# Kernel optimization log

Hardware: AMD Instinct MI355X
Metric: run time of the kernel (lower is better)

Reference implementation:

```python
import jax, jax.numpy as jnp
import numpy as np
from jax import lax

G0, G1 = 16, 16
UNITS = 256


def setup_inputs() -> dict:
    key = jax.random.key(0)
    ks = jax.random.split(key, 20)
    B, H, W, C = 64, 512, 512, 3
    U = UNITS
    flat = 12 * 12 * 3  # after two VALID 3x3 convs on 16x16x3
    inp = {
        'image': jax.random.normal(ks[0], (B, H, W, C), jnp.float32),
        'section': jax.random.uniform(ks[1], (B, 3), jnp.float32),
        'h0': jax.random.normal(ks[2], (B, U), jnp.float32) * 0.1,
        'c0': jax.random.normal(ks[3], (B, U), jnp.float32) * 0.1,
        'conv1_k': jax.random.normal(ks[4], (3, 3, C, 3), jnp.float32) * 0.2,
        'conv1_b': jnp.zeros((3,), jnp.float32),
        'conv2_k': jax.random.normal(ks[5], (3, 3, 3, 3), jnp.float32) * 0.2,
        'conv2_b': jnp.zeros((3,), jnp.float32),
        'dense_w': jax.random.normal(ks[6], (flat, U), jnp.float32) * (1.0 / np.sqrt(flat)),
        'dense_b': jnp.zeros((U,), jnp.float32),
        'lstm_k': jax.random.normal(ks[7], (U, 4 * U), jnp.float32) * (1.0 / np.sqrt(U)),
        'lstm_rk': jax.random.normal(ks[8], (U, 4 * U), jnp.float32) * (1.0 / np.sqrt(U)),
        'lstm_b': jnp.zeros((4 * U,), jnp.float32),
        'nsc_w1': jax.random.normal(ks[9], (U, U), jnp.float32) * (1.0 / np.sqrt(U)),
        'nsc_b1': jnp.zeros((U,), jnp.float32),
        'nsc_w2': jax.random.normal(ks[10], (U, 3), jnp.float32) * (1.0 / np.sqrt(U)),
        'nsc_b2': jnp.zeros((3,), jnp.float32),
    }
    return inp


def _interpolate(image, section):
    # image: (B,H,W,C); section: (B,3) = (x, y, scale); coords in [0,1],
    # mapped linearly onto grid indices with constant (clamp) extension,
    # matching tfp.math.batch_interp_regular_nd_grid over image axes 1,2.
    B, H, W, C = image.shape
    starts = section[:, :2]                       # (B,2)
    stops = section[:, :2] + section[:, 2:]       # (B,2) broadcast scale
    t0 = jnp.linspace(0.0, 1.0, G0)               # along grid_dim[0]
    alpha = jnp.linspace(0.0, 1.0, G1)            # along grid_dim[1]
    # p0[b,i,j]: coordinate mapped to image axis 1 (H)
    p0 = (starts[:, 0, None] + t0[None, :] * (stops[:, 0] - starts[:, 0])[:, None])[:, :, None]
    p0 = jnp.broadcast_to(p0, (B, G0, G1))
    # p1[b,i,j]: coordinate mapped to image axis 2 (W)
    p1 = (starts[:, 1, None] + alpha[None, :] * (stops[:, 1] - starts[:, 1])[:, None])[:, None, :]
    p1 = jnp.broadcast_to(p1, (B, G0, G1))
    fy = jnp.clip(p0 * (H - 1), 0.0, H - 1)
    fx = jnp.clip(p1 * (W - 1), 0.0, W - 1)
    y0 = jnp.floor(fy).astype(jnp.int32)
    x0 = jnp.floor(fx).astype(jnp.int32)
    y1 = jnp.minimum(y0 + 1, H - 1)
    x1 = jnp.minimum(x0 + 1, W - 1)
    wy = (fy - y0)[..., None]
    wx = (fx - x0)[..., None]
    b = jnp.arange(B)[:, None, None]
    v00 = image[b, y0, x0]
    v01 = image[b, y0, x1]
    v10 = image[b, y1, x0]
    v11 = image[b, y1, x1]
    top = v00 * (1 - wx) + v01 * wx
    bot = v10 * (1 - wx) + v11 * wx
    return top * (1 - wy) + bot * wy            # (B,G0,G1,C)


def _conv_relu(x, k, b):
    y = lax.conv_general_dilated(x, k, (1, 1), 'VALID',
                                 dimension_numbers=('NHWC', 'HWIO', 'NHWC'))
    return jax.nn.relu(y + b)


def reference(image, section, h0, c0, conv1_k, conv1_b, conv2_k, conv2_b,
              dense_w, dense_b, lstm_k, lstm_rk, lstm_b,
              nsc_w1, nsc_b1, nsc_w2, nsc_b2):
    sec = _interpolate(image, section)                 # (B,16,16,C)
    x = _conv_relu(sec, conv1_k, conv1_b)              # (B,14,14,3)
    x = _conv_relu(x, conv2_k, conv2_b)                # (B,12,12,3)
    x = x.reshape(x.shape[0], -1)                      # (B,432)
    x = jax.nn.relu(x @ dense_w + dense_b)             # (B,U)
    # Keras LSTMCell: gate order i, f, g(c), o
    z = x @ lstm_k + h0 @ lstm_rk + lstm_b
    i, f, g, o = jnp.split(z, 4, axis=-1)
    c_new = jax.nn.sigmoid(f) * c0 + jax.nn.sigmoid(i) * jnp.tanh(g)
    h_new = jax.nn.sigmoid(o) * jnp.tanh(c_new)
    nsc = jax.nn.relu(h_new @ nsc_w1 + nsc_b1)
    next_section = jax.nn.sigmoid(nsc @ nsc_w2 + nsc_b2)  # (B,3)
    return h_new, c_new, next_section
```

## Files before the change

kernel.cpp:

```cpp
#include <hip/hip_runtime.h>
#include <math.h>

#define BATCH 64
#define IMH 512
#define IMW 512
#define UNITS 256

__device__ __forceinline__ float sigmoidf_(float x) {
    return 1.0f / (1.0f + __expf(-x));
}
__device__ __forceinline__ float tanhf_(float x) {
    float e = __expf(2.0f * x);
    return 1.0f - 2.0f / (e + 1.0f);
}

#define WS_X   0
#define WS_Z   16384
#define WS_NSC (16384 + 65536)

__global__ __launch_bounds__(512) void k1_front(
    const float* __restrict__ image, const float* __restrict__ section,
    const float* __restrict__ k1, const float* __restrict__ b1,
    const float* __restrict__ k2, const float* __restrict__ b2,
    const float* __restrict__ dw, const float* __restrict__ db,
    float* __restrict__ ws)
{
    const int b   = blockIdx.x;
    const int tid = threadIdx.x;

    __shared__ float s_sec[16][16][3];
    __shared__ float s_c1[14][14][3];
    __shared__ float s_flat[432];
    __shared__ float s_pf[2048];
    __shared__ float s_k1[84];
    __shared__ float s_k2[84];

    if (tid < 81)       s_k1[tid]      = k1[tid];
    else if (tid < 84)  s_k1[tid]      = b1[tid - 81];
    else if (tid < 165) s_k2[tid - 84] = k2[tid - 84];
    else if (tid < 168) s_k2[tid - 84] = b2[tid - 165];

    if (tid < 256) {
        const float s0 = section[b * 3 + 0];
        const float s1 = section[b * 3 + 1];
        const float s2 = section[b * 3 + 2];
        const int i = tid >> 4, j = tid & 15;
        float p0 = s0 + (float)i * (1.0f / 15.0f) * s2;
        float p1 = s1 + (float)j * (1.0f / 15.0f) * s2;
        float fy = fminf(fmaxf(p0 * 511.0f, 0.0f), 511.0f);
        float fx = fminf(fmaxf(p1 * 511.0f, 0.0f), 511.0f);
        int y0 = (int)floorf(fy);
        int x0 = (int)floorf(fx);
        int y1 = min(y0 + 1, 511);
        int x1 = min(x0 + 1, 511);
        float wy = fy - (float)y0;
        float wx = fx - (float)x0;
        const float* base = image + (size_t)b * IMH * IMW * 3;
        const float* p00 = base + (y0 * IMW + x0) * 3;
        const float* p01 = base + (y0 * IMW + x1) * 3;
        const float* p10 = base + (y1 * IMW + x0) * 3;
        const float* p11 = base + (y1 * IMW + x1) * 3;
        #pragma unroll
        for (int c = 0; c < 3; ++c) {
            float top = p00[c] * (1.0f - wx) + p01[c] * wx;
            float bot = p10[c] * (1.0f - wx) + p11[c] * wx;
            s_sec[i][j][c] = top * (1.0f - wy) + bot * wy;
        }
    }
    __syncthreads();

    if (tid < 196) {
        const int i = tid / 14, j = tid % 14;
        float a0 = s_k1[81], a1 = s_k1[82], a2 = s_k1[83];
        #pragma unroll
        for (int di = 0; di < 3; ++di)
            #pragma unroll
            for (int dj = 0; dj < 3; ++dj)
                #pragma unroll
                for (int ci = 0; ci < 3; ++ci) {
                    float v = s_sec[i + di][j + dj][ci];
                    const int kb = ((di * 3 + dj) * 3 + ci) * 3;
                    a0 += v * s_k1[kb + 0];
                    a1 += v * s_k1[kb + 1];
                    a2 += v * s_k1[kb + 2];
                }
        s_c1[i][j][0] = fmaxf(a0, 0.0f);
        s_c1[i][j][1] = fmaxf(a1, 0.0f);
        s_c1[i][j][2] = fmaxf(a2, 0.0f);
    }
    __syncthreads();

    if (tid < 144) {
        const int i = tid / 12, j = tid % 12;
        float a0 = s_k2[81], a1 = s_k2[82], a2 = s_k2[83];
        #pragma unroll
        for (int di = 0; di < 3; ++di)
            #pragma unroll
            for (int dj = 0; dj < 3; ++dj)
                #pragma unroll
                for (int ci = 0; ci < 3; ++ci) {
                    float v = s_c1[i + di][j + dj][ci];
                    const int kb = ((di * 3 + dj) * 3 + ci) * 3;
                    a0 += v * s_k2[kb + 0];
                    a1 += v * s_k2[kb + 1];
                    a2 += v * s_k2[kb + 2];
                }
        const int fb = tid * 3;
        s_flat[fb + 0] = fmaxf(a0, 0.0f);
        s_flat[fb + 1] = fmaxf(a1, 0.0f);
        s_flat[fb + 2] = fmaxf(a2, 0.0f);
    }
    __syncthreads();

    {
        const int ks = tid >> 6;
        const int q  = tid & 63;
        const int k0 = ks * 54;
        const float4* wp = (const float4*)dw + (size_t)k0 * 64 + q;
        const float* fp = s_flat + k0;
        float4 acc = {0.f, 0.f, 0.f, 0.f};
        #pragma unroll 18
        for (int k = 0; k < 54; ++k) {
            const float4 w = wp[k * 64];
            const float v = fp[k];
            acc.x += v * w.x; acc.y += v * w.y; acc.z += v * w.z; acc.w += v * w.w;
        }
        ((float4*)s_pf)[ks * 64 + q] = acc;
    }
    __syncthreads();
    if (tid < 256) {
        const int q2 = tid >> 2, comp = tid & 3;
        float a = db[tid];
        #pragma unroll
        for (int ks2 = 0; ks2 < 8; ++ks2)
            a += s_pf[(ks2 * 64 + q2) * 4 + comp];
        ws[WS_X + b * 256 + tid] = fmaxf(a, 0.0f);
    }
}

__global__ __launch_bounds__(256) void k2_lstm_gemm(
    const float* __restrict__ h0, const float* __restrict__ lk,
    const float* __restrict__ lrk, const float* __restrict__ lb,
    float* __restrict__ ws)
{
    const int bx    = blockIdx.x;
    const int ct    = bx & 15;
    const int bt    = bx >> 4;
    const int col0  = ct * 64;
    const int colq0 = ct * 16;
    const int row0  = bt * 4;
    const int tid   = threadIdx.x;

    __shared__ float s_x4[4][256];
    __shared__ float s_h4[4][256];
    __shared__ float s_zpf[1024];

    for (int i = tid; i < 1024; i += 256) {
        const int r = i >> 8, k = i & 255;
        s_x4[r][k] = ws[WS_X + (row0 + r) * 256 + k];
        s_h4[r][k] = h0[(row0 + r) * 256 + k];
    }
    __syncthreads();

    {
        const int q  = tid & 15;
        const int bb = (tid >> 4) & 3;
        const int ks = tid >> 6;
        const int k0 = ks * 64;
        const float4* lkp = (const float4*)lk  + (size_t)k0 * 256 + colq0 + q;
        const float4* lrp = (const float4*)lrk + (size_t)k0 * 256 + colq0 + q;
        const float* xp = s_x4[bb] + k0;
        const float* hp = s_h4[bb] + k0;
        float4 acc = {0.f, 0.f, 0.f, 0.f};
        #pragma unroll 16
        for (int k = 0; k < 64; ++k) {
            const float4 a = lkp[k * 256];
            const float4 r = lrp[k * 256];
            const float xv = xp[k];
            const float hv = hp[k];
            acc.x += xv * a.x + hv * r.x;
            acc.y += xv * a.y + hv * r.y;
            acc.z += xv * a.z + hv * r.z;
            acc.w += xv * a.w + hv * r.w;
        }
        ((float4*)s_zpf)[(ks * 4 + bb) * 16 + q] = acc;
    }
    __syncthreads();

    {
        const int c   = tid & 63;
        const int bb2 = tid >> 6;
        const int q2 = c >> 2, comp = c & 3;
        float z = lb[col0 + c];
        #pragma unroll
        for (int ks2 = 0; ks2 < 4; ++ks2)
            z += s_zpf[((ks2 * 4 + bb2) * 16 + q2) * 4 + comp];
        ws[WS_Z + (row0 + bb2) * 1024 + col0 + c] = z;
    }
}

__global__ __launch_bounds__(256) void k3_cell_nsc1(
    const float* __restrict__ c0, const float* __restrict__ w1,
    const float* __restrict__ nb1, float* __restrict__ ws,
    float* __restrict__ out)
{
    const int bx    = blockIdx.x;
    const int ct    = bx & 3;
    const int bt    = bx >> 2;
    const int col0  = ct * 64;
    const int colq0 = ct * 16;
    const int row0  = bt * 2;
    const int tid   = threadIdx.x;

    __shared__ float s_hn[2][256];
    __shared__ float s_pf[1024];

    {
        const int u = tid;
        #pragma unroll
        for (int b2 = 0; b2 < 2; ++b2) {
            const int row = row0 + b2;
            const float zi = ws[WS_Z + row * 1024 + u];
            const float zf = ws[WS_Z + row * 1024 + 256 + u];
            const float zg = ws[WS_Z + row * 1024 + 512 + u];
            const float zo = ws[WS_Z + row * 1024 + 768 + u];
            const float cprev = c0[row * 256 + u];
            const float cn = sigmoidf_(zf) * cprev + sigmoidf_(zi) * tanhf_(zg);
            const float hn = sigmoidf_(zo) * tanhf_(cn);
            s_hn[b2][u] = hn;
            if (ct == 0) {
                out[row * 256 + u] = hn;
                out[BATCH * UNITS + row * 256 + u] = cn;
            }
        }
    }
    __syncthreads();

    {
        const int q  = tid & 15;
        const int bb = (tid >> 4) & 1;
        const int ks = tid >> 5;
        const int k0 = ks * 32;
        const float4* wp = (const float4*)w1 + (size_t)k0 * 64 + colq0 + q;
        const float* hp = s_hn[bb] + k0;
        float4 acc = {0.f, 0.f, 0.f, 0.f};
        #pragma unroll 16
        for (int k = 0; k < 32; ++k) {
            const float4 w = wp[k * 64];
            const float v = hp[k];
            acc.x += v * w.x; acc.y += v * w.y; acc.z += v * w.z; acc.w += v * w.w;
        }
        ((float4*)s_pf)[(ks * 2 + bb) * 16 + q] = acc;
    }
    __syncthreads();

    if (tid < 128) {
        const int c   = tid & 63;
        const int bb2 = tid >> 6;
        const int q2 = c >> 2, comp = c & 3;
        float a = nb1[col0 + c];
        #pragma unroll
        for (int ks2 = 0; ks2 < 8; ++ks2)
            a += s_pf[((ks2 * 2 + bb2) * 16 + q2) * 4 + comp];
        ws[WS_NSC + (row0 + bb2) * 256 + col0 + c] = fmaxf(a, 0.0f);
    }
}

__global__ __launch_bounds__(192) void k4_nsc2(
    const float* __restrict__ w2, const float* __restrict__ nb2,
    const float* __restrict__ ws, float* __restrict__ out)
{
    const int b   = blockIdx.x;
    const int tid = threadIdx.x;
    const int j = tid >> 6;
    const int l = tid & 63;
    float p = 0.0f;
    #pragma unroll
    for (int k = l; k < 256; k += 64)
        p += ws[WS_NSC + b * 256 + k] * w2[k * 3 + j];
    #pragma unroll
    for (int off = 32; off > 0; off >>= 1)
        p += __shfl_down(p, off);
    if (l == 0)
        out[2 * BATCH * UNITS + b * 3 + j] = sigmoidf_(p + nb2[j]);
}

extern "C" void kernel_launch(void* const* d_in, const int* in_sizes, int n_in,
                              void* d_out, int out_size, void* d_ws, size_t ws_size,
                              hipStream_t stream) {
    const float* image   = (const float*)d_in[0];
    const float* section = (const float*)d_in[1];
    const float* h0      = (const float*)d_in[2];
    const float* c0      = (const float*)d_in[3];
    const float* k1      = (const float*)d_in[4];
    const float* b1      = (const float*)d_in[5];
    const float* k2      = (const float*)d_in[6];
    const float* b2      = (const float*)d_in[7];
    const float* dw      = (const float*)d_in[8];
    const float* db      = (const float*)d_in[9];
    const float* lk      = (const float*)d_in[10];
    const float* lrk     = (const float*)d_in[11];
    const float* lb      = (const float*)d_in[12];
    const float* w1      = (const float*)d_in[13];
    const float* nb1     = (const float*)d_in[14];
    const float* w2      = (const float*)d_in[15];
    const float* nb2     = (const float*)d_in[16];
    float* out = (float*)d_out;
    float* ws  = (float*)d_ws;

    k1_front<<<64, 512, 0, stream>>>(image, section, k1, b1, k2, b2, dw, db, ws);
    k2_lstm_gemm<<<256, 256, 0, stream>>>(h0, lk, lrk, lb, ws);
    k3_cell_nsc1<<<128, 256, 0, stream>>>(c0, w1, nb1, ws, out);
    k4_nsc2<<<64, 192, 0, stream>>>(w2, nb2, ws, out);
}
```

Before: 302.6 us.

## Fuse four kernels into one cooperative kernel with grid syncs

Replaces the four separate launches (front conv/dense, LSTM GEMM, cell+nsc1, nsc2) with a single cooperative kernel of 256 blocks that uses grid.sync between phases. The cell, nsc1 and nsc2 stages are merged per batch row into one block, so the NSC intermediate stays in shared memory instead of going through the workspace. The front stage now runs with 256 threads instead of 512. The aim is to remove launch overhead and inter-kernel gaps. In exchange it adds grid-wide barrier cost, leaves most blocks idle in the per-batch phases, and the union of shared buffers raises per-block LDS use.

```diff
diff --git a/kernel.cpp b/kernel.cpp
--- a/kernel.cpp
+++ b/kernel.cpp
@@ -1,5 +1,8 @@
 #include <hip/hip_runtime.h>
+#include <hip/hip_cooperative_groups.h>
 #include <math.h>
+
+namespace cg = cooperative_groups;
 
 #define BATCH 64
 #define IMH 512
@@ -14,275 +17,254 @@
     return 1.0f - 2.0f / (e + 1.0f);
 }
 
-#define WS_X   0
-#define WS_Z   16384
-#define WS_NSC (16384 + 65536)
-
-__global__ __launch_bounds__(512) void k1_front(
+#define WS_X 0
+#define WS_Z 16384
+
+__global__ __launch_bounds__(256) void fused_coop(
     const float* __restrict__ image, const float* __restrict__ section,
+    const float* __restrict__ h0, const float* __restrict__ c0,
     const float* __restrict__ k1, const float* __restrict__ b1,
     const float* __restrict__ k2, const float* __restrict__ b2,
     const float* __restrict__ dw, const float* __restrict__ db,
+    const float* __restrict__ lk, const float* __restrict__ lrk,
+    const float* __restrict__ lb, const float* __restrict__ w1,
+    const float* __restrict__ nb1, const float* __restrict__ w2,
+    const float* __restrict__ nb2, float* __restrict__ out,
     float* __restrict__ ws)
 {
-    const int b   = blockIdx.x;
+    cg::grid_group grid = cg::this_grid();
+    const int bx  = blockIdx.x;
     const int tid = threadIdx.x;
 
     __shared__ float s_sec[16][16][3];
     __shared__ float s_c1[14][14][3];
     __shared__ float s_flat[432];
-    __shared__ float s_pf[2048];
     __shared__ float s_k1[84];
     __shared__ float s_k2[84];
-
-    if (tid < 81)       s_k1[tid]      = k1[tid];
-    else if (tid < 84)  s_k1[tid]      = b1[tid - 81];
-    else if (tid < 165) s_k2[tid - 84] = k2[tid - 84];
-    else if (tid < 168) s_k2[tid - 84] = b2[tid - 165];
-
-    if (tid < 256) {
-        const float s0 = section[b * 3 + 0];
-        const float s1 = section[b * 3 + 1];
-        const float s2 = section[b * 3 + 2];
-        const int i = tid >> 4, j = tid & 15;
-        float p0 = s0 + (float)i * (1.0f / 15.0f) * s2;
-        float p1 = s1 + (float)j * (1.0f / 15.0f) * s2;
-        float fy = fminf(fmaxf(p0 * 511.0f, 0.0f), 511.0f);
-        float fx = fminf(fmaxf(p1 * 511.0f, 0.0f), 511.0f);
-        int y0 = (int)floorf(fy);
-        int x0 = (int)floorf(fx);
-        int y1 = min(y0 + 1, 511);
-        int x1 = min(x0 + 1, 511);
-        float wy = fy - (float)y0;
-        float wx = fx - (float)x0;
-        const float* base = image + (size_t)b * IMH * IMW * 3;
-        const float* p00 = base + (y0 * IMW + x0) * 3;
-        const float* p01 = base + (y0 * IMW + x1) * 3;
-        const float* p10 = base + (y1 * IMW + x0) * 3;
-        const float* p11 = base + (y1 * IMW + x1) * 3;
-        #pragma unroll
-        for (int c = 0; c < 3; ++c) {
-            float top = p00[c] * (1.0f - wx) + p01[c] * wx;
-            float bot = p10[c] * (1.0f - wx) + p11[c] * wx;
-            s_sec[i][j][c] = top * (1.0f - wy) + bot * wy;
-        }
-    }
-    __syncthreads();
-
-    if (tid < 196) {
-        const int i = tid / 14, j = tid % 14;
-        float a0 = s_k1[81], a1 = s_k1[82], a2 = s_k1[83];
-        #pragma unroll
-        for (int di = 0; di < 3; ++di)
-            #pragma unroll
-            for (int dj = 0; dj < 3; ++dj)
-                #pragma unroll
-                for (int ci = 0; ci < 3; ++ci) {
-                    float v = s_sec[i + di][j + dj][ci];
-                    const int kb = ((di * 3 + dj) * 3 + ci) * 3;
-                    a0 += v * s_k1[kb + 0];
-                    a1 += v * s_k1[kb + 1];
-                    a2 += v * s_k1[kb + 2];
-                }
-        s_c1[i][j][0] = fmaxf(a0, 0.0f);
-        s_c1[i][j][1] = fmaxf(a1, 0.0f);
-        s_c1[i][j][2] = fmaxf(a2, 0.0f);
-    }
-    __syncthreads();
-
-    if (tid < 144) {
-        const int i = tid / 12, j = tid % 12;
-        float a0 = s_k2[81], a1 = s_k2[82], a2 = s_k2[83];
-        #pragma unroll
-        for (int di = 0; di < 3; ++di)
-            #pragma unroll
-            for (int dj = 0; dj < 3; ++dj)
-                #pragma unroll
-                for (int ci = 0; ci < 3; ++ci) {
-                    float v = s_c1[i + di][j + dj][ci];
-                    const int kb = ((di * 3 + dj) * 3 + ci) * 3;
-                    a0 += v * s_k2[kb + 0];
-                    a1 += v * s_k2[kb + 1];
-                    a2 += v * s_k2[kb + 2];
-                }
-        const int fb = tid * 3;
-        s_flat[fb + 0] = fmaxf(a0, 0.0f);
-        s_flat[fb + 1] = fmaxf(a1, 0.0f);
-        s_flat[fb + 2] = fmaxf(a2, 0.0f);
-    }
-    __syncthreads();
-
-    {
-        const int ks = tid >> 6;
-        const int q  = tid & 63;
-        const int k0 = ks * 54;
-        const float4* wp = (const float4*)dw + (size_t)k0 * 64 + q;
-        const float* fp = s_flat + k0;
-        float4 acc = {0.f, 0.f, 0.f, 0.f};
-        #pragma unroll 18
-        for (int k = 0; k < 54; ++k) {
-            const float4 w = wp[k * 64];
-            const float v = fp[k];
-            acc.x += v * w.x; acc.y += v * w.y; acc.z += v * w.z; acc.w += v * w.w;
-        }
-        ((float4*)s_pf)[ks * 64 + q] = acc;
-    }
-    __syncthreads();
-    if (tid < 256) {
-        const int q2 = tid >> 2, comp = tid & 3;
-        float a = db[tid];
-        #pragma unroll
-        for (int ks2 = 0; ks2 < 8; ++ks2)
-            a += s_pf[(ks2 * 64 + q2) * 4 + comp];
-        ws[WS_X + b * 256 + tid] = fmaxf(a, 0.0f);
-    }
-}
-
-__global__ __launch_bounds__(256) void k2_lstm_gemm(
-    const float* __restrict__ h0, const float* __restrict__ lk,
-    const float* __restrict__ lrk, const float* __restrict__ lb,
-    float* __restrict__ ws)
-{
-    const int bx    = blockIdx.x;
-    const int ct    = bx & 15;
-    const int bt    = bx >> 4;
-    const int col0  = ct * 64;
-    const int colq0 = ct * 16;
-    const int row0  = bt * 4;
-    const int tid   = threadIdx.x;
-
+    __shared__ float s_pf[1024];
     __shared__ float s_x4[4][256];
     __shared__ float s_h4[4][256];
     __shared__ float s_zpf[1024];
-
-    for (int i = tid; i < 1024; i += 256) {
-        const int r = i >> 8, k = i & 255;
-        s_x4[r][k] = ws[WS_X + (row0 + r) * 256 + k];
-        s_h4[r][k] = h0[(row0 + r) * 256 + k];
+    __shared__ float s_hn[256];
+    __shared__ float s_nsc[256];
+
+    if (bx < 64) {
+        const int b = bx;
+
+        if (tid < 81)       s_k1[tid]      = k1[tid];
+        else if (tid < 84)  s_k1[tid]      = b1[tid - 81];
+        else if (tid < 165) s_k2[tid - 84] = k2[tid - 84];
+        else if (tid < 168) s_k2[tid - 84] = b2[tid - 165];
+
+        {
+            const float s0 = section[b * 3 + 0];
+            const float s1 = section[b * 3 + 1];
+            const float s2 = section[b * 3 + 2];
+            const int i = tid >> 4, j = tid & 15;
+            float p0 = s0 + (float)i * (1.0f / 15.0f) * s2;
+            float p1 = s1 + (float)j * (1.0f / 15.0f) * s2;
+            float fy = fminf(fmaxf(p0 * 511.0f, 0.0f), 511.0f);
+            float fx = fminf(fmaxf(p1 * 511.0f, 0.0f), 511.0f);
+            int y0 = (int)floorf(fy);
+            int x0 = (int)floorf(fx);
+            int y1 = min(y0 + 1, 511);
+            int x1 = min(x0 + 1, 511);
+            float wy = fy - (float)y0;
+            float wx = fx - (float)x0;
+            const float* base = image + (size_t)b * IMH * IMW * 3;
+            const float* p00 = base + (y0 * IMW + x0) * 3;
+            const float* p01 = base + (y0 * IMW + x1) * 3;
+            const float* p10 = base + (y1 * IMW + x0) * 3;
+            const float* p11 = base + (y1 * IMW + x1) * 3;
+            #pragma unroll
+            for (int c = 0; c < 3; ++c) {
+                float top = p00[c] * (1.0f - wx) + p01[c] * wx;
+                float bot = p10[c] * (1.0f - wx) + p11[c] * wx;
+                s_sec[i][j][c] = top * (1.0f - wy) + bot * wy;
+            }
+        }
+        __syncthreads();
+
+        if (tid < 196) {
+            const int i = tid / 14, j = tid % 14;
+            float a0 = s_k1[81], a1 = s_k1[82], a2 = s_k1[83];
+            #pragma unroll
+            for (int di = 0; di < 3; ++di)
+                #pragma unroll
+                for (int dj = 0; dj < 3; ++dj)
+                    #pragma unroll
+                    for (int ci = 0; ci < 3; ++ci) {
+                        float v = s_sec[i + di][j + dj][ci];
+                        const int kb = ((di * 3 + dj) * 3 + ci) * 3;
+                        a0 += v * s_k1[kb + 0];
+                        a1 += v * s_k1[kb + 1];
+                        a2 += v * s_k1[kb + 2];
+                    }
+            s_c1[i][j][0] = fmaxf(a0, 0.0f);
+            s_c1[i][j][1] = fmaxf(a1, 0.0f);
+            s_c1[i][j][2] = fmaxf(a2, 0.0f);
+        }
+        __syncthreads();
+
+        if (tid < 144) {
+            const int i = tid / 12, j = tid % 12;
+            float a0 = s_k2[81], a1 = s_k2[82], a2 = s_k2[83];
+            #pragma unroll
+            for (int di = 0; di < 3; ++di)
+                #pragma unroll
+                for (int dj = 0; dj < 3; ++dj)
+                    #pragma unroll
+                    for (int ci = 0; ci < 3; ++ci) {
+                        float v = s_c1[i + di][j + dj][ci];
+                        const int kb = ((di * 3 + dj) * 3 + ci) * 3;
+                        a0 += v * s_k2[kb + 0];
+                        a1 += v * s_k2[kb + 1];
+                        a2 += v * s_k2[kb + 2];
+                    }
+            const int fb = tid * 3;
+            s_flat[fb + 0] = fmaxf(a0, 0.0f);
+            s_flat[fb + 1] = fmaxf(a1, 0.0f);
+            s_flat[fb + 2] = fmaxf(a2, 0.0f);
+        }
+        __syncthreads();
+
+        {
+            const int ks = tid >> 6;
+            const int q  = tid & 63;
+            const int k0 = ks * 108;
+            const float4* wp = (const float4*)dw + (size_t)k0 * 64 + q;
+            const float* fp = s_flat + k0;
+            float4 acc = {0.f, 0.f, 0.f, 0.f};
+            #pragma unroll 27
+            for (int k = 0; k < 108; ++k) {
+                const float4 w = wp[k * 64];
+                const float v = fp[k];
+                acc.x += v * w.x; acc.y += v * w.y; acc.z += v * w.z; acc.w += v * w.w;
+            }
+            ((float4*)s_pf)[ks * 64 + q] = acc;
+        }
+        __syncthreads();
+        {
+            float a = db[tid];
+            #pragma unroll
+            for (int ks2 = 0; ks2 < 4; ++ks2)
+                a += s_pf[ks2 * 256 + tid];
+            ws[WS_X + b * 256 + tid] = fmaxf(a, 0.0f);
+        }
     }
-    __syncthreads();
+
+    grid.sync();
 
     {
-        const int q  = tid & 15;
-        const int bb = (tid >> 4) & 3;
-        const int ks = tid >> 6;
-        const int k0 = ks * 64;
-        const float4* lkp = (const float4*)lk  + (size_t)k0 * 256 + colq0 + q;
-        const float4* lrp = (const float4*)lrk + (size_t)k0 * 256 + colq0 + q;
-        const float* xp = s_x4[bb] + k0;
-        const float* hp = s_h4[bb] + k0;
-        float4 acc = {0.f, 0.f, 0.f, 0.f};
-        #pragma unroll 16
-        for (int k = 0; k < 64; ++k) {
-            const float4 a = lkp[k * 256];
-            const float4 r = lrp[k * 256];
-            const float xv = xp[k];
-            const float hv = hp[k];
-            acc.x += xv * a.x + hv * r.x;
-            acc.y += xv * a.y + hv * r.y;
-            acc.z += xv * a.z + hv * r.z;
-            acc.w += xv * a.w + hv * r.w;
-        }
-        ((float4*)s_zpf)[(ks * 4 + bb) * 16 + q] = acc;
+        const int ct    = bx & 15;
+        const int bt    = bx >> 4;
+        const int col0  = ct * 64;
+        const int colq0 = ct * 16;
+        const int row0  = bt * 4;
+
+        for (int i = tid; i < 1024; i += 256) {
+            const int r = i >> 8, k = i & 255;
+            s_x4[r][k] = ws[WS_X + (row0 + r) * 256 + k];
+            s_h4[r][k] = h0[(row0 + r) * 256 + k];
+        }
+        __syncthreads();
+
+        {
+            const int q  = tid & 15;
+            const int bb = (tid >> 4) & 3;
+            const int ks = tid >> 6;
+            const int k0 = ks * 64;
+            const float4* lkp = (const float4*)lk  + (size_t)k0 * 256 + colq0 + q;
+            const float4* lrp = (const float4*)lrk + (size_t)k0 * 256 + colq0 + q;
+            const float* xp = s_x4[bb] + k0;
+            const float* hp = s_h4[bb] + k0;
+            float4 acc = {0.f, 0.f, 0.f, 0.f};
+            #pragma unroll 16
+            for (int k = 0; k < 64; ++k) {
+                const float4 a = lkp[k * 256];
+                const float4 r = lrp[k * 256];
+                const float xv = xp[k];
+                const float hv = hp[k];
+                acc.x += xv * a.x + hv * r.x;
+                acc.y += xv * a.y + hv * r.y;
+                acc.z += xv * a.z + hv * r.z;
+                acc.w += xv * a.w + hv * r.w;
+            }
+            ((float4*)s_zpf)[(ks * 4 + bb) * 16 + q] = acc;
+        }
+        __syncthreads();
+
+        {
+            const int c   = tid & 63;
+            const int bb2 = tid >> 6;
+            const int q2 = c >> 2, comp = c & 3;
+            float z = lb[col0 + c];
+            #pragma unroll
+            for (int ks2 = 0; ks2 < 4; ++ks2)
+                z += s_zpf[((ks2 * 4 + bb2) * 16 + q2) * 4 + comp];
+            ws[WS_Z + (row0 + bb2) * 1024 + col0 + c] = z;
+        }
     }
-    __syncthreads();
-
-    {
-        const int c   = tid & 63;
-        const int bb2 = tid >> 6;
-        const int q2 = c >> 2, comp = c & 3;
-        float z = lb[col0 + c];
-        #pragma unroll
-        for (int ks2 = 0; ks2 < 4; ++ks2)
-            z += s_zpf[((ks2 * 4 + bb2) * 16 + q2) * 4 + comp];
-        ws[WS_Z + (row0 + bb2) * 1024 + col0 + c] = z;
-    }
-}
-
-__global__ __launch_bounds__(256) void k3_cell_nsc1(
-    const float* __restrict__ c0, const float* __restrict__ w1,
-    const float* __restrict__ nb1, float* __restrict__ ws,
-    float* __restrict__ out)
-{
-    const int bx    = blockIdx.x;
-    const int ct    = bx & 3;
-    const int bt    = bx >> 2;
-    const int col0  = ct * 64;
-    const int colq0 = ct * 16;
-    const int row0  = bt * 2;
-    const int tid   = threadIdx.x;
-
-    __shared__ float s_hn[2][256];
-    __shared__ float s_pf[1024];
-
-    {
-        const int u = tid;
-        #pragma unroll
-        for (int b2 = 0; b2 < 2; ++b2) {
-            const int row = row0 + b2;
-            const float zi = ws[WS_Z + row * 1024 + u];
-            const float zf = ws[WS_Z + row * 1024 + 256 + u];
-            const float zg = ws[WS_Z + row * 1024 + 512 + u];
-            const float zo = ws[WS_Z + row * 1024 + 768 + u];
-            const float cprev = c0[row * 256 + u];
+
+    grid.sync();
+
+    if (bx < 64) {
+        const int b = bx;
+
+        {
+            const int u = tid;
+            const float zi = ws[WS_Z + b * 1024 + u];
+            const float zf = ws[WS_Z + b * 1024 + 256 + u];
+            const float zg = ws[WS_Z + b * 1024 + 512 + u];
+            const float zo = ws[WS_Z + b * 1024 + 768 + u];
+            const float cprev = c0[b * 256 + u];
             const float cn = sigmoidf_(zf) * cprev + sigmoidf_(zi) * tanhf_(zg);
             const float hn = sigmoidf_(zo) * tanhf_(cn);
-            s_hn[b2][u] = hn;
-            if (ct == 0) {
-                out[row * 256 + u] = hn;
-                out[BATCH * UNITS + row * 256 + u] = cn;
+            out[b * 256 + u] = hn;
+            out[BATCH * UNITS + b * 256 + u] = cn;
+            s_hn[u] = hn;
+        }
+        __syncthreads();
+
+        {
+            const int ks = tid >> 6;
+            const int q  = tid & 63;
+            const int k0 = ks * 64;
+            const float4* wp = (const float4*)w1 + (size_t)k0 * 64 + q;
+            const float* hp = s_hn + k0;
+            float4 acc = {0.f, 0.f, 0.f, 0.f};
+            #pragma unroll 16
+            for (int k = 0; k < 64; ++k) {
+                const float4 w = wp[k * 64];
+                const float v = hp[k];
+                acc.x += v * w.x; acc.y += v * w.y; acc.z += v * w.z; acc.w += v * w.w;
             }
+            ((float4*)s_pf)[ks * 64 + q] = acc;
+        }
+        __syncthreads();
+        {
+            float a = nb1[tid];
+            #pragma unroll
+            for (int ks2 = 0; ks2 < 4; ++ks2)
+                a += s_pf[ks2 * 256 + tid];
+            s_nsc[tid] = fmaxf(a, 0.0f);
+        }
+        __syncthreads();
+
+        if (tid < 192) {
+            const int j = tid >> 6;
+            const int l = tid & 63;
+            float p = 0.0f;
+            #pragma unroll
+            for (int k = l; k < 256; k += 64)
+                p += s_nsc[k] * w2[k * 3 + j];
+            #pragma unroll
+            for (int off = 32; off > 0; off >>= 1)
+                p += __shfl_down(p, off);
+            if (l == 0)
+                out[2 * BATCH * UNITS + b * 3 + j] = sigmoidf_(p + nb2[j]);
         }
     }
-    __syncthreads();
-
-    {
-        const int q  = tid & 15;
-        const int bb = (tid >> 4) & 1;
-        const int ks = tid >> 5;
-        const int k0 = ks * 32;
-        const float4* wp = (const float4*)w1 + (size_t)k0 * 64 + colq0 + q;
-        const float* hp = s_hn[bb] + k0;
-        float4 acc = {0.f, 0.f, 0.f, 0.f};
-        #pragma unroll 16
-        for (int k = 0; k < 32; ++k) {
-            const float4 w = wp[k * 64];
-            const float v = hp[k];
-            acc.x += v * w.x; acc.y += v * w.y; acc.z += v * w.z; acc.w += v * w.w;
-        }
-        ((float4*)s_pf)[(ks * 2 + bb) * 16 + q] = acc;
-    }
-    __syncthreads();
-
-    if (tid < 128) {
-        const int c   = tid & 63;
-        const int bb2 = tid >> 6;
-        const int q2 = c >> 2, comp = c & 3;
-        float a = nb1[col0 + c];
-        #pragma unroll
-        for (int ks2 = 0; ks2 < 8; ++ks2)
-            a += s_pf[((ks2 * 2 + bb2) * 16 + q2) * 4 + comp];
-        ws[WS_NSC + (row0 + bb2) * 256 + col0 + c] = fmaxf(a, 0.0f);
-    }
-}
-
-__global__ __launch_bounds__(192) void k4_nsc2(
-    const float* __restrict__ w2, const float* __restrict__ nb2,
-    const float* __restrict__ ws, float* __restrict__ out)
-{
-    const int b   = blockIdx.x;
-    const int tid = threadIdx.x;
-    const int j = tid >> 6;
-    const int l = tid & 63;
-    float p = 0.0f;
-    #pragma unroll
-    for (int k = l; k < 256; k += 64)
-        p += ws[WS_NSC + b * 256 + k] * w2[k * 3 + j];
-    #pragma unroll
-    for (int off = 32; off > 0; off >>= 1)
-        p += __shfl_down(p, off);
-    if (l == 0)
-        out[2 * BATCH * UNITS + b * 3 + j] = sigmoidf_(p + nb2[j]);
 }
 
 extern "C" void kernel_launch(void* const* d_in, const int* in_sizes, int n_in,
@@ -308,8 +290,13 @@
     float* out = (float*)d_out;
     float* ws  = (float*)d_ws;
 
-    k1_front<<<64, 512, 0, stream>>>(image, section, k1, b1, k2, b2, dw, db, ws);
-    k2_lstm_gemm<<<256, 256, 0, stream>>>(h0, lk, lrk, lb, ws);
-    k3_cell_nsc1<<<128, 256, 0, stream>>>(c0, w1, nb1, ws, out);
-    k4_nsc2<<<64, 192, 0, stream>>>(w2, nb2, ws, out);
+    void* args[] = {
+        (void*)&image, (void*)&section, (void*)&h0, (void*)&c0,
+        (void*)&k1, (void*)&b1, (void*)&k2, (void*)&b2,
+        (void*)&dw, (void*)&db, (void*)&lk, (void*)&lrk, (void*)&lb,
+        (void*)&w1, (void*)&nb1, (void*)&w2, (void*)&nb2,
+        (void*)&out, (void*)&ws
+    };
+    hipLaunchCooperativeKernel((const void*)fused_coop,
+                               dim3(256), dim3(256), args, 0, stream);
 }
```

Measured after the change: 367.4 us. 1.21x slower.
